# Kernel optimization log

Measured on AMD Instinct MI355X. Metric: run time of the kernel, lower is better.

Reference implementation:

```python
import jax, jax.numpy as jnp
import numpy as np
import math

N_FILT = 80
FILT_DIM = 251
FS = 16000
MIN_FREQ = 50.0
MIN_BAND = 50.0


def _init_params():
    low_freq_mel = 80.0
    high_freq_mel = 2595.0 * np.log10(1.0 + FS / 2.0 / 700.0)
    mel_points = np.linspace(low_freq_mel, high_freq_mel, N_FILT)
    f_cos = 700.0 * (10.0 ** (mel_points / 2595.0) - 1.0)
    b1 = np.roll(f_cos, 1)
    b2 = np.roll(f_cos, -1)
    b1[0] = 30.0
    b2[-1] = FS / 2.0 - 100.0
    freq_scale = FS * 1.0
    return (jnp.asarray(b1 / freq_scale, dtype=jnp.float32),
            jnp.asarray((b2 - b1) / freq_scale, dtype=jnp.float32))


def setup_inputs() -> dict:
    key = jax.random.key(0)
    x = jax.random.normal(key, (32, 1, 32000), dtype=jnp.float32)
    filt_b1, filt_band = _init_params()
    return {"x": x, "filt_b1": filt_b1, "filt_band": filt_band}


def _sinc_batch(band, t_right):
    # band: [F] (in Hz, already scaled by fs); t_right: [T] (seconds)
    arg = 2.0 * math.pi * band[:, None] * t_right[None, :]  # [F, T]
    y_right = jnp.sin(arg) / arg
    y_left = y_right[:, ::-1]
    ones = jnp.ones((band.shape[0], 1), dtype=band.dtype)
    return jnp.concatenate([y_left, ones, y_right], axis=1)  # [F, 2T+1]


def _build_filters(filt_b1, filt_band):
    N = FILT_DIM
    freq_scale = float(FS)
    t_right = (jnp.linspace(1.0, (N - 1) / 2.0, (N - 1) // 2) / FS).astype(jnp.float32)
    filt_beg = jnp.abs(filt_b1) + MIN_FREQ / freq_scale            # [F]
    filt_end = filt_beg + (jnp.abs(filt_band) + MIN_BAND / freq_scale)
    # torch.linspace(0, N, steps=N): N points from 0 to N inclusive
    n = jnp.linspace(0.0, float(N), N).astype(jnp.float32)
    window = (0.54 - 0.46 * jnp.cos(2.0 * math.pi * n / N)).astype(jnp.float32)
    low_pass1 = 2.0 * filt_beg[:, None] * _sinc_batch(filt_beg * freq_scale, t_right)
    low_pass2 = 2.0 * filt_end[:, None] * _sinc_batch(filt_end * freq_scale, t_right)
    band_pass = low_pass2 - low_pass1                              # [F, N]
    band_pass = band_pass / jnp.max(band_pass, axis=1, keepdims=True)
    return band_pass * window[None, :]                             # [F, N]


def reference(x, filt_b1, filt_band):
    filters = _build_filters(filt_b1, filt_band)                   # [N_filt, Filt_dim]
    out = jax.lax.conv_general_dilated(
        x, filters[:, None, :],
        window_strides=(1,), padding='VALID',
        dimension_numbers=('NCH', 'OIH', 'NCH'))
    return out  # [B, N_filt, L - Filt_dim + 1]
```

## Files before the change

### kernel.cpp

```cpp
#include <hip/hip_runtime.h>
#include <math.h>

#define N_FILT   80
#define FILT_DIM 251
#define KPAD     256
#define SIG_LEN  32000
#define OUT_LEN  31750
#define BATCH    32
#define TPB      320

#define STRIP    1024
#define LROW4    644
#define OBS2     36

#define TWO_PI_F 6.28318530717958647692f

typedef __attribute__((ext_vector_type(8))) short    short8;
typedef __attribute__((ext_vector_type(8))) _Float16 half8;
typedef __attribute__((ext_vector_type(4))) float    float4v;
typedef __attribute__((ext_vector_type(2))) float    float2v;
typedef __attribute__((ext_vector_type(2))) unsigned uint2v;
typedef __attribute__((ext_vector_type(4))) unsigned uint4v;

__global__ __launch_bounds__(256) void build_filters_kernel(
    const float* __restrict__ b1, const float* __restrict__ band,
    unsigned short* __restrict__ fh)
{
    const int f = blockIdx.x;
    const int i = threadIdx.x;

    const float MINF = 50.0f / 16000.0f;
    const float fb = fabsf(b1[f]) + MINF;
    const float fe = fb + fabsf(band[f]) + MINF;

    float v = 0.0f;
    if (i < FILT_DIM) {
        int m = i - 125; m = (m < 0) ? -m : m;
        if (m == 0) v = 2.0f * fe - 2.0f * fb;
        else {
            float a1 = TWO_PI_F * fb * (float)m;
            float a2 = TWO_PI_F * fe * (float)m;
            v = 2.0f * fe * (sinf(a2) / a2) - 2.0f * fb * (sinf(a1) / a1);
        }
    }

    __shared__ float red[256];
    red[i] = (i < FILT_DIM) ? v : -INFINITY;
    __syncthreads();
    #pragma unroll
    for (int s = 128; s > 0; s >>= 1) {
        if (i < s) red[i] = fmaxf(red[i], red[i + s]);
        __syncthreads();
    }
    const float mx = red[0];

    const float w   = 0.54f - 0.46f * cosf(TWO_PI_F * (float)i / 250.0f);
    const float val = (i < FILT_DIM) ? (v / mx) * w : 0.0f;
    const _Float16 h = (_Float16)val;
    fh[f * KPAD + i] = __builtin_bit_cast(unsigned short, h);
}

__global__ __launch_bounds__(TPB, 8) void sinc_mfma_kernel(
    const float* __restrict__ x,
    const unsigned short* __restrict__ fh,
    float* __restrict__ out)
{
    __shared__ __align__(16) unsigned xf[4 * LROW4];
    __shared__ __align__(16) float    ob[5][16 * OBS2];

    const int tid = threadIdx.x;
    const unsigned raw = blockIdx.x;
    const unsigned swz = (raw & 7u) * 128u + (raw >> 3);
    const int strip = (int)(swz & 31u);
    const int n     = (int)(swz >> 5);
    const int e0    = strip * STRIP;
    const float* xp = x + (size_t)n * SIG_LEN;

    for (int d = tid; d < LROW4; d += TPB) {
        const int g = e0 + 2 * d;
        float v0, v1, v2, v3, v4;
        if (g + 4 < SIG_LEN) {
            float2 p01 = *(const float2*)(xp + g);
            float2 p23 = *(const float2*)(xp + g + 2);
            v0 = p01.x; v1 = p01.y; v2 = p23.x; v3 = p23.y; v4 = xp[g + 4];
        } else {
            v0 = (g     < SIG_LEN) ? xp[g]     : 0.0f;
            v1 = (g + 1 < SIG_LEN) ? xp[g + 1] : 0.0f;
            v2 = (g + 2 < SIG_LEN) ? xp[g + 2] : 0.0f;
            v3 = (g + 3 < SIG_LEN) ? xp[g + 3] : 0.0f;
            v4 = (g + 4 < SIG_LEN) ? xp[g + 4] : 0.0f;
        }
        const _Float16 h0 = (_Float16)v0, h1 = (_Float16)v1, h2 = (_Float16)v2;
        const _Float16 h3 = (_Float16)v3, h4 = (_Float16)v4;
        union { _Float16 h[2]; unsigned u; } p0, p1, p2, p3;
        p0.h[0] = h0; p0.h[1] = h1;
        p1.h[0] = h1; p1.h[1] = h2;
        p2.h[0] = h2; p2.h[1] = h3;
        p3.h[0] = h3; p3.h[1] = h4;
        xf[0 * LROW4 + d] = p0.u;
        xf[1 * LROW4 + d] = p1.u;
        xf[2 * LROW4 + d] = p2.u;
        xf[3 * LROW4 + d] = p3.u;
    }

    const int lane = tid & 63;
    const int w    = tid >> 6;
    const int m    = lane & 15;
    const int q    = lane >> 4;
    short8 Ah[8];
    {
        const unsigned short* ph = fh + (w * 16 + m) * KPAD + q * 8;
        #pragma unroll
        for (int kb = 0; kb < 8; ++kb)
            Ah[kb] = *(const short8*)(ph + kb * 32);
    }
    __syncthreads();

    const int r = m & 3;
    const unsigned base = (unsigned)(r * LROW4 + 2 * (m >> 2) + 4 * q);

    float* const obw  = &ob[w][0];
    const int    cp   = 2 * (lane & 15);
    const int    rr0  = lane >> 4;
    const size_t row0 = ((size_t)n * N_FILT + w * 16) * OUT_LEN;

    for (int gp = 0; gp < 32; ++gp) {
        #pragma unroll
        for (int tl = 0; tl < 2; ++tl) {
            const int tt = gp * 2 + tl;
            float4v a0 = {0.f,0.f,0.f,0.f}, a1 = {0.f,0.f,0.f,0.f};
            const unsigned o0 = base + 8u * (unsigned)tt;
            #pragma unroll
            for (int kk = 0; kk < 4; ++kk) {
                const unsigned oa = o0 + 32u * kk;
                const unsigned ob_ = oa + 16u;
                const uint2v a_lo = *(const uint2v*)(&xf[oa]);
                const uint2v a_hi = *(const uint2v*)(&xf[oa + 2]);
                const uint2v b_lo = *(const uint2v*)(&xf[ob_]);
                const uint2v b_hi = *(const uint2v*)(&xf[ob_ + 2]);
                const uint4v fa = {a_lo.x, a_lo.y, a_hi.x, a_hi.y};
                const uint4v fb = {b_lo.x, b_lo.y, b_hi.x, b_hi.y};
                a0 = __builtin_amdgcn_mfma_f32_16x16x32_f16(
                         __builtin_bit_cast(half8, Ah[2*kk]),
                         __builtin_bit_cast(half8, fa), a0, 0, 0, 0);
                a1 = __builtin_amdgcn_mfma_f32_16x16x32_f16(
                         __builtin_bit_cast(half8, Ah[2*kk+1]),
                         __builtin_bit_cast(half8, fb), a1, 0, 0, 0);
            }
            const int oc = tl * 16 + m;
            #pragma unroll
            for (int rg = 0; rg < 4; ++rg)
                obw[(q * 4 + rg) * OBS2 + oc] = a0[rg] + a1[rg];
        }

        const int t0 = e0 + gp * 32 + cp;
        if (t0 + 1 < OUT_LEN) {
            #pragma unroll
            for (int j = 0; j < 4; ++j) {
                const int row = j * 4 + rr0;
                const float2v v = *(const float2v*)(&obw[row * OBS2 + cp]);
                *(float2v*)(out + row0 + (size_t)row * OUT_LEN + t0) = v;
            }
        }
    }
}

extern "C" void kernel_launch(void* const* d_in, const int* in_sizes, int n_in,
                              void* d_out, int out_size, void* d_ws, size_t ws_size,
                              hipStream_t stream)
{
    const float* x    = (const float*)d_in[0];
    const float* b1   = (const float*)d_in[1];
    const float* band = (const float*)d_in[2];
    float* outp = (float*)d_out;

    unsigned short* fh = (unsigned short*)d_ws;

    build_filters_kernel<<<dim3(N_FILT), dim3(256), 0, stream>>>(b1, band, fh);

    dim3 grid(1024);
    sinc_mfma_kernel<<<grid, dim3(TPB), 0, stream>>>(x, fh, outp);
}
```

Before: 103.1 us.

## Align output row stores to 256B boundaries with double-buffered LDS staging

The output staging now covers 64 columns per group and is double-buffered. Each row's stores are shifted by a per-row offset so that lanes write fully aligned 64-float segments, even though OUT_LEN=31750 leaves row starts misaligned. The goal is to cut partial or misaligned cache-line writes on the dominant output-write traffic. In exchange, LDS use per block grows and launch bounds drop to 5 blocks per SM, which may lower occupancy; stores also become scalar per lane instead of float2.

```diff
diff --git a/kernel.cpp b/kernel.cpp
--- a/kernel.cpp
+++ b/kernel.cpp
@@ -11,14 +11,12 @@
 
 #define STRIP    1024
 #define LROW4    644
-#define OBS2     36
 
 #define TWO_PI_F 6.28318530717958647692f
 
 typedef __attribute__((ext_vector_type(8))) short    short8;
 typedef __attribute__((ext_vector_type(8))) _Float16 half8;
 typedef __attribute__((ext_vector_type(4))) float    float4v;
-typedef __attribute__((ext_vector_type(2))) float    float2v;
 typedef __attribute__((ext_vector_type(2))) unsigned uint2v;
 typedef __attribute__((ext_vector_type(4))) unsigned uint4v;
 
@@ -60,13 +58,13 @@
     fh[f * KPAD + i] = __builtin_bit_cast(unsigned short, h);
 }
 
-__global__ __launch_bounds__(TPB, 8) void sinc_mfma_kernel(
+__global__ __launch_bounds__(TPB, 5) void sinc_mfma_kernel(
     const float* __restrict__ x,
     const unsigned short* __restrict__ fh,
     float* __restrict__ out)
 {
     __shared__ __align__(16) unsigned xf[4 * LROW4];
-    __shared__ __align__(16) float    ob[5][16 * OBS2];
+    __shared__ __align__(16) float    ob[5][2][16][66];
 
     const int tid = threadIdx.x;
     const unsigned raw = blockIdx.x;
@@ -116,53 +114,82 @@
     }
     __syncthreads();
 
-    const int r = m & 3;
-    const unsigned base = (unsigned)(r * LROW4 + 2 * (m >> 2) + 4 * q);
-
-    float* const obw  = &ob[w][0];
-    const int    cp   = 2 * (lane & 15);
-    const int    rr0  = lane >> 4;
-    const size_t row0 = ((size_t)n * N_FILT + w * 16) * OUT_LEN;
-
-    for (int gp = 0; gp < 32; ++gp) {
+    const int r4 = m & 3;
+    const unsigned base = (unsigned)(r4 * LROW4 + 2 * (m >> 2) + 4 * q);
+
+    float (*obw)[16][66] = ob[w];
+    const int    fgbase  = n * N_FILT + w * 16;
+    const size_t rowbase = (size_t)fgbase * OUT_LEN;
+
+    #define COMPUTE_GROUP(gv)                                                  \
+    {                                                                          \
+        const int h_ = (gv) & 1;                                               \
+        _Pragma("unroll")                                                      \
+        for (int tl = 0; tl < 4; ++tl) {                                       \
+            const int tt = (gv) * 4 + tl;                                      \
+            float4v a0 = {0.f,0.f,0.f,0.f}, a1 = {0.f,0.f,0.f,0.f};            \
+            const unsigned o0 = base + 8u * (unsigned)tt;                      \
+            _Pragma("unroll")                                                  \
+            for (int kk = 0; kk < 4; ++kk) {                                   \
+                const unsigned oa = o0 + 32u * kk;                             \
+                const uint2v alo = *(const uint2v*)(&xf[oa]);                  \
+                const uint2v ahi = *(const uint2v*)(&xf[oa + 2]);              \
+                const uint2v blo = *(const uint2v*)(&xf[oa + 16]);             \
+                const uint2v bhi = *(const uint2v*)(&xf[oa + 18]);             \
+                const uint4v fa  = {alo.x, alo.y, ahi.x, ahi.y};               \
+                const uint4v fbv = {blo.x, blo.y, bhi.x, bhi.y};               \
+                a0 = __builtin_amdgcn_mfma_f32_16x16x32_f16(                   \
+                         __builtin_bit_cast(half8, Ah[2*kk]),                  \
+                         __builtin_bit_cast(half8, fa),  a0, 0, 0, 0);         \
+                a1 = __builtin_amdgcn_mfma_f32_16x16x32_f16(                   \
+                         __builtin_bit_cast(half8, Ah[2*kk+1]),                \
+                         __builtin_bit_cast(half8, fbv), a1, 0, 0, 0);         \
+            }                                                                  \
+            const int oc = tl * 16 + m;                                        \
+            _Pragma("unroll")                                                  \
+            for (int rg = 0; rg < 4; ++rg)                                     \
+                obw[h_][q * 4 + rg][oc] = a0[rg] + a1[rg];                     \
+        }                                                                      \
+    }
+
+    COMPUTE_GROUP(0);
+    #pragma unroll
+    for (int j = 0; j < 16; ++j) {
+        const int sh = (64 - ((6 * (fgbase + j)) & 63)) & 63;
+        if (lane < sh) {
+            const int t = e0 + lane;
+            if (t < OUT_LEN)
+                out[rowbase + (size_t)j * OUT_LEN + t] = obw[0][j][lane];
+        }
+    }
+
+    for (int k = 0; k < 15; ++k) {
+        COMPUTE_GROUP(k + 1);
+        const int hk = k & 1;
         #pragma unroll
-        for (int tl = 0; tl < 2; ++tl) {
-            const int tt = gp * 2 + tl;
-            float4v a0 = {0.f,0.f,0.f,0.f}, a1 = {0.f,0.f,0.f,0.f};
-            const unsigned o0 = base + 8u * (unsigned)tt;
-            #pragma unroll
-            for (int kk = 0; kk < 4; ++kk) {
-                const unsigned oa = o0 + 32u * kk;
-                const unsigned ob_ = oa + 16u;
-                const uint2v a_lo = *(const uint2v*)(&xf[oa]);
-                const uint2v a_hi = *(const uint2v*)(&xf[oa + 2]);
-                const uint2v b_lo = *(const uint2v*)(&xf[ob_]);
-                const uint2v b_hi = *(const uint2v*)(&xf[ob_ + 2]);
-                const uint4v fa = {a_lo.x, a_lo.y, a_hi.x, a_hi.y};
-                const uint4v fb = {b_lo.x, b_lo.y, b_hi.x, b_hi.y};
-                a0 = __builtin_amdgcn_mfma_f32_16x16x32_f16(
-                         __builtin_bit_cast(half8, Ah[2*kk]),
-                         __builtin_bit_cast(half8, fa), a0, 0, 0, 0);
-                a1 = __builtin_amdgcn_mfma_f32_16x16x32_f16(
-                         __builtin_bit_cast(half8, Ah[2*kk+1]),
-                         __builtin_bit_cast(half8, fb), a1, 0, 0, 0);
-            }
-            const int oc = tl * 16 + m;
-            #pragma unroll
-            for (int rg = 0; rg < 4; ++rg)
-                obw[(q * 4 + rg) * OBS2 + oc] = a0[rg] + a1[rg];
-        }
-
-        const int t0 = e0 + gp * 32 + cp;
-        if (t0 + 1 < OUT_LEN) {
-            #pragma unroll
-            for (int j = 0; j < 4; ++j) {
-                const int row = j * 4 + rr0;
-                const float2v v = *(const float2v*)(&obw[row * OBS2 + cp]);
-                *(float2v*)(out + row0 + (size_t)row * OUT_LEN + t0) = v;
-            }
-        }
-    }
+        for (int j = 0; j < 16; ++j) {
+            const int sh = (64 - ((6 * (fgbase + j)) & 63)) & 63;
+            const int sl = sh + lane;
+            const int cl = sl & 63;
+            const int hb = (sl < 64) ? hk : (hk ^ 1);
+            const float v = obw[hb][j][cl];
+            const int t = e0 + 64 * k + sl;
+            if (t < OUT_LEN)
+                out[rowbase + (size_t)j * OUT_LEN + t] = v;
+        }
+    }
+
+    #pragma unroll
+    for (int j = 0; j < 16; ++j) {
+        const int sh = (64 - ((6 * (fgbase + j)) & 63)) & 63;
+        const int sl = sh + lane;
+        if (sl < 64) {
+            const int t = e0 + 960 + sl;
+            if (t < OUT_LEN)
+                out[rowbase + (size_t)j * OUT_LEN + t] = obw[1][j][sl];
+        }
+    }
+    #undef COMPUTE_GROUP
 }
 
 extern "C" void kernel_launch(void* const* d_in, const int* in_sizes, int n_in,
```

Result: slower. 145.2 us (+40.9%).
